# Optimization experiments

Hardware: AMD Instinct MI355X
Metric: run time of the kernel (lower is better)

## Reference

```python
import jax, jax.numpy as jnp
import numpy as np

B, N, C_IN, C_OUT = 4, 2048, 1024, 1024


def setup_inputs() -> dict:
    key = jax.random.key(0)
    ks = jax.random.split(key, 4)
    scale = 1.0 / np.sqrt(C_IN)
    return {
        "hidden_states": jax.random.normal(ks[0], (B, N, C_IN), dtype=jnp.float32),
        "Wq": jax.random.normal(ks[1], (C_OUT, C_IN), dtype=jnp.float32) * scale,
        "bq": jnp.zeros((C_OUT,), dtype=jnp.float32),
        "Wk": jax.random.normal(ks[2], (C_OUT, C_IN), dtype=jnp.float32) * scale,
        "bk": jnp.zeros((C_OUT,), dtype=jnp.float32),
        "Wv": jax.random.normal(ks[3], (C_OUT, C_IN), dtype=jnp.float32) * scale,
        "bv": jnp.zeros((C_OUT,), dtype=jnp.float32),
    }


def reference(hidden_states, Wq, bq, Wk, bk, Wv, bv):
    # torch nn.Linear: y = x @ W.T + b
    Q = jnp.einsum("bnc,dc->bnd", hidden_states, Wq) + bq
    K = jnp.einsum("bnc,dc->bnd", hidden_states, Wk) + bk
    V = jnp.einsum("bnc,dc->bnd", hidden_states, Wv) + bv
    d_k = K.shape[-1]
    scores = jnp.einsum("bnd,bmd->bnm", Q, K) * (d_k ** -0.5)  # [B,N,N]
    attention = jax.nn.softmax(scores, axis=-1)
    out = jnp.einsum("bnm,bmd->bnd", attention, V)
    return (out, attention)
```

## Files before the change

### kernel.cpp

```cpp
#include <hip/hip_runtime.h>
#include <cstdint>

typedef __attribute__((ext_vector_type(8))) short bf16x8;
typedef __attribute__((ext_vector_type(4))) float f32x4;

__device__ __forceinline__ unsigned short f2bf(float v) {
  unsigned u = __builtin_bit_cast(unsigned, v);
  u += 0x7FFFu + ((u >> 16) & 1u);
  return (unsigned short)(u >> 16);
}

__device__ __forceinline__ void gload16(const unsigned short* g, unsigned short* l) {
  __builtin_amdgcn_global_load_lds(
      (const __attribute__((address_space(1))) void*)(uintptr_t)g,
      (__attribute__((address_space(3))) void*)(uint32_t)(uintptr_t)l,
      16, 0, 0);
}

__device__ __forceinline__ void gemm_core(
    const unsigned short* __restrict__ A, const unsigned short* __restrict__ B,
    int lda, int ldb, int K,
    unsigned short* ldsA, unsigned short* ldsB, f32x4 acc[4][4])
{
  const int tid  = threadIdx.x;
  const int wave = tid >> 6;
  const int lane = tid & 63;
  const int wm = (wave >> 1) * 64;
  const int wn = (wave & 1) * 64;
  const int lrow = lane & 15;
  const int kq = lane >> 4;

  const int sr = lane >> 3;
  const int sc = (lane & 7) ^ (sr & 7);
  const unsigned short* ga = A + (long)(wave * 32 + sr) * lda + sc * 8;
  const unsigned short* gb = B + (long)(wave * 32 + sr) * ldb + sc * 8;
  unsigned short* lA = ldsA + wave * 2048;
  unsigned short* lB = ldsB + wave * 2048;

  const int pc0 = ((0 * 4 + kq) ^ (lrow & 7)) * 8;
  const int pc1 = ((1 * 4 + kq) ^ (lrow & 7)) * 8;

#pragma unroll 1
  for (int kb = 0; kb < K; kb += 64) {
    __syncthreads();
#pragma unroll
    for (int i = 0; i < 4; ++i) {
      gload16(ga + kb + (long)i * 8 * lda, lA + i * 512);
      gload16(gb + kb + (long)i * 8 * ldb, lB + i * 512);
    }
    __syncthreads();

    bf16x8 af[4], bfr[4];
#pragma unroll
    for (int i = 0; i < 4; ++i)
      af[i] = *(const bf16x8*)(ldsA + (wm + i * 16 + lrow) * 64 + pc0);
#pragma unroll
    for (int j = 0; j < 4; ++j)
      bfr[j] = *(const bf16x8*)(ldsB + (wn + j * 16 + lrow) * 64 + pc0);
#pragma unroll
    for (int i = 0; i < 4; ++i)
#pragma unroll
      for (int j = 0; j < 4; ++j)
        acc[i][j] = __builtin_amdgcn_mfma_f32_16x16x32_bf16(af[i], bfr[j], acc[i][j], 0, 0, 0);

#pragma unroll
    for (int i = 0; i < 4; ++i)
      af[i] = *(const bf16x8*)(ldsA + (wm + i * 16 + lrow) * 64 + pc1);
#pragma unroll
    for (int j = 0; j < 4; ++j)
      bfr[j] = *(const bf16x8*)(ldsB + (wn + j * 16 + lrow) * 64 + pc1);
#pragma unroll
    for (int i = 0; i < 4; ++i)
#pragma unroll
      for (int j = 0; j < 4; ++j)
        acc[i][j] = __builtin_amdgcn_mfma_f32_16x16x32_bf16(af[i], bfr[j], acc[i][j], 0, 0, 0);
  }
}

__global__ __launch_bounds__(256, 4) void gemm_qkv(
    const unsigned short* __restrict__ xh,
    const unsigned short* __restrict__ wh,
    const float* __restrict__ bq, const float* __restrict__ bk, const float* __restrict__ bv,
    unsigned short* __restrict__ Qh, unsigned short* __restrict__ Kh,
    unsigned short* __restrict__ Vth)
{
  __shared__ __align__(16) unsigned short ldsA[8192];
  __shared__ __align__(16) unsigned short ldsB[8192];
  const int Mblk = blockIdx.x * 128;
  const int sel  = blockIdx.y >> 3;
  const int nb   = blockIdx.y & 7;

  const unsigned short* A = xh + (long)Mblk * 1024;
  const unsigned short* B = wh + sel * 1048576 + (long)(nb * 128) * 1024;
  const float* bias = (sel == 0) ? bq : (sel == 1) ? bk : bv;

  f32x4 acc[4][4] = {};
  gemm_core(A, B, 1024, 1024, 1024, ldsA, ldsB, acc);

  const int lane = threadIdx.x & 63, wave = threadIdx.x >> 6;
  const int wm = (wave >> 1) * 64, wn = (wave & 1) * 64;
  const int lrow = lane & 15, kq = lane >> 4;

#pragma unroll
  for (int i = 0; i < 4; ++i) {
#pragma unroll
    for (int j = 0; j < 4; ++j) {
      const int col = nb * 128 + wn + j * 16 + lrow;
      const float bsv = bias[col];
#pragma unroll
      for (int r = 0; r < 4; ++r) {
        const int tok = Mblk + wm + i * 16 + kq * 4 + r;
        const unsigned short h = f2bf(acc[i][j][r] + bsv);
        if (sel == 2) {
          Vth[(long)(tok >> 11) * 2097152 + (long)col * 2048 + (tok & 2047)] = h;
        } else if (sel == 0) {
          Qh[(long)tok * 1024 + col] = h;
        } else {
          Kh[(long)tok * 1024 + col] = h;
        }
      }
    }
  }
}

__global__ __launch_bounds__(256, 4) void gemm_f32out(
    const unsigned short* __restrict__ A, const unsigned short* __restrict__ B,
    int lda, int ldb, int K,
    long sA, long sB, float* __restrict__ C, int ldc, long sC, float alpha)
{
  __shared__ __align__(16) unsigned short ldsA[8192];
  __shared__ __align__(16) unsigned short ldsB[8192];
  const int Mblk = blockIdx.x * 128;
  const int Nblk = blockIdx.y * 128;
  const long z = blockIdx.z;
  const unsigned short* Ab = A + z * sA + (long)Mblk * lda;
  const unsigned short* Bb = B + z * sB + (long)Nblk * ldb;
  float* Cb = C + z * sC;

  f32x4 acc[4][4] = {};
  gemm_core(Ab, Bb, lda, ldb, K, ldsA, ldsB, acc);

  const int lane = threadIdx.x & 63, wave = threadIdx.x >> 6;
  const int wm = (wave >> 1) * 64, wn = (wave & 1) * 64;
  const int lrow = lane & 15, kq = lane >> 4;
#pragma unroll
  for (int i = 0; i < 4; ++i)
#pragma unroll
    for (int j = 0; j < 4; ++j)
#pragma unroll
      for (int r = 0; r < 4; ++r) {
        const int row = Mblk + wm + i * 16 + kq * 4 + r;
        const int col = Nblk + wn + j * 16 + lrow;
        Cb[(long)row * ldc + col] = alpha * acc[i][j][r];
      }
}

__global__ __launch_bounds__(256) void softmax_rows(
    float* __restrict__ S, unsigned short* __restrict__ Ph)
{
  __shared__ float red[4];
  const long row = blockIdx.x;
  float* rp = S + row * 2048;
  const int t = threadIdx.x;

  float x[8];
  *(float4*)&x[0] = reinterpret_cast<const float4*>(rp)[t];
  *(float4*)&x[4] = reinterpret_cast<const float4*>(rp)[t + 256];

  float m = x[0];
#pragma unroll
  for (int i = 1; i < 8; ++i) m = fmaxf(m, x[i]);
  for (int o = 32; o; o >>= 1) m = fmaxf(m, __shfl_xor(m, o, 64));
  if ((t & 63) == 0) red[t >> 6] = m;
  __syncthreads();
  m = fmaxf(fmaxf(red[0], red[1]), fmaxf(red[2], red[3]));
  __syncthreads();

  float s = 0.f;
#pragma unroll
  for (int i = 0; i < 8; ++i) { x[i] = expf(x[i] - m); s += x[i]; }
  for (int o = 32; o; o >>= 1) s += __shfl_xor(s, o, 64);
  if ((t & 63) == 0) red[t >> 6] = s;
  __syncthreads();
  s = (red[0] + red[1]) + (red[2] + red[3]);
  const float inv = 1.0f / s;

#pragma unroll
  for (int i = 0; i < 8; ++i) x[i] *= inv;
  reinterpret_cast<float4*>(rp)[t]       = *(float4*)&x[0];
  reinterpret_cast<float4*>(rp)[t + 256] = *(float4*)&x[4];

  const long b0 = row * 2048 + t * 4;
#pragma unroll
  for (int k = 0; k < 4; ++k) Ph[b0 + k] = f2bf(x[k]);
  const long b1 = row * 2048 + 1024 + t * 4;
#pragma unroll
  for (int k = 0; k < 4; ++k) Ph[b1 + k] = f2bf(x[4 + k]);
}

__global__ __launch_bounds__(256) void to_bf16(
    const float* __restrict__ x, unsigned short* __restrict__ hi, int n)
{
  int i = blockIdx.x * 256 + threadIdx.x;
  const int stride = gridDim.x * 256;
  for (; i < n; i += stride) hi[i] = f2bf(x[i]);
}

extern "C" void kernel_launch(void* const* d_in, const int* in_sizes, int n_in,
                              void* d_out, int out_size, void* d_ws, size_t ws_size,
                              hipStream_t stream)
{
  const float* x  = (const float*)d_in[0];
  const float* Wq = (const float*)d_in[1];
  const float* bq = (const float*)d_in[2];
  const float* Wk = (const float*)d_in[3];
  const float* bk = (const float*)d_in[4];
  const float* Wv = (const float*)d_in[5];
  const float* bv = (const float*)d_in[6];

  float* out  = (float*)d_out;
  float* attn = (float*)d_out + 8388608;

  unsigned short* ws  = (unsigned short*)d_ws;
  unsigned short* xh  = ws;
  unsigned short* wh  = xh + 8388608;
  unsigned short* Qh  = wh + 3145728;
  unsigned short* Kh  = Qh + 8388608;
  unsigned short* Vth = Kh + 8388608;
  unsigned short* Ph  = Vth + 8388608;

  to_bf16<<<4096, 256, 0, stream>>>(x, xh, 8388608);
  to_bf16<<<512, 256, 0, stream>>>(Wq, wh, 1048576);
  to_bf16<<<512, 256, 0, stream>>>(Wk, wh + 1048576, 1048576);
  to_bf16<<<512, 256, 0, stream>>>(Wv, wh + 2097152, 1048576);

  gemm_qkv<<<dim3(64, 24), 256, 0, stream>>>(xh, wh, bq, bk, bv, Qh, Kh, Vth);

  gemm_f32out<<<dim3(16, 16, 4), 256, 0, stream>>>(Qh, Kh, 1024, 1024, 1024,
      2097152L, 2097152L, attn, 2048, 4194304L, 0.03125f);

  softmax_rows<<<8192, 256, 0, stream>>>(attn, Ph);

  gemm_f32out<<<dim3(16, 8, 4), 256, 0, stream>>>(Ph, Vth, 2048, 2048, 2048,
      4194304L, 2097152L, out, 1024, 2097152L, 1.0f);
}
```

Measured before the change: 314.2 us.

## Rewrite GEMM core as 8-wave 128x256 tile with double-buffered LDS prefetch

Replaces the 4-wave 128x128 GEMM core with an 8-wave 128x256 block tile. It uses a double-buffered LDS pipeline where global-to-LDS loads for the next A and B tiles are issued while MFMAs run on the current tile, with manual vmcnt waits, raw barriers and setprio around the MFMA bursts. This is meant to hide global load latency that the old load/sync/compute loop exposed, and to raise reuse per block. The bf16 conversion kernel is also vectorised to float4 loads. It raises LDS use (96KB per block) and relies on hand-placed waitcnt and barriers, so any ordering mistake risks races; there are also fewer blocks per launch.

Result: slower. 321.6 us (+2.3%).

```diff
diff --git a/kernel.cpp b/kernel.cpp
--- a/kernel.cpp
+++ b/kernel.cpp
@@ -17,99 +17,145 @@
       16, 0, 0);
 }
 
+#define BAR()   asm volatile("s_barrier" ::: "memory")
+#define LGKM0() asm volatile("s_waitcnt lgkmcnt(0)" ::: "memory")
+#define VM4()   asm volatile("s_waitcnt vmcnt(4)" ::: "memory")
+#define VM0()   asm volatile("s_waitcnt vmcnt(0)" ::: "memory")
+
 __device__ __forceinline__ void gemm_core(
     const unsigned short* __restrict__ A, const unsigned short* __restrict__ B,
-    int lda, int ldb, int K,
-    unsigned short* ldsA, unsigned short* ldsB, f32x4 acc[4][4])
+    int lda, int ldb, int NT,
+    unsigned short* lds, f32x4 acc[4][4])
 {
   const int tid  = threadIdx.x;
-  const int wave = tid >> 6;
+  const int w    = tid >> 6;
   const int lane = tid & 63;
-  const int wm = (wave >> 1) * 64;
-  const int wn = (wave & 1) * 64;
+  const int wr   = w >> 2;
+  const int wc   = w & 3;
   const int lrow = lane & 15;
-  const int kq = lane >> 4;
-
-  const int sr = lane >> 3;
-  const int sc = (lane & 7) ^ (sr & 7);
-  const unsigned short* ga = A + (long)(wave * 32 + sr) * lda + sc * 8;
-  const unsigned short* gb = B + (long)(wave * 32 + sr) * ldb + sc * 8;
-  unsigned short* lA = ldsA + wave * 2048;
-  unsigned short* lB = ldsB + wave * 2048;
-
-  const int pc0 = ((0 * 4 + kq) ^ (lrow & 7)) * 8;
-  const int pc1 = ((1 * 4 + kq) ^ (lrow & 7)) * 8;
-
-#pragma unroll 1
-  for (int kb = 0; kb < K; kb += 64) {
-    __syncthreads();
-#pragma unroll
-    for (int i = 0; i < 4; ++i) {
-      gload16(ga + kb + (long)i * 8 * lda, lA + i * 512);
-      gload16(gb + kb + (long)i * 8 * ldb, lB + i * 512);
-    }
-    __syncthreads();
-
-    bf16x8 af[4], bfr[4];
-#pragma unroll
-    for (int i = 0; i < 4; ++i)
-      af[i] = *(const bf16x8*)(ldsA + (wm + i * 16 + lrow) * 64 + pc0);
-#pragma unroll
-    for (int j = 0; j < 4; ++j)
-      bfr[j] = *(const bf16x8*)(ldsB + (wn + j * 16 + lrow) * 64 + pc0);
-#pragma unroll
-    for (int i = 0; i < 4; ++i)
-#pragma unroll
-      for (int j = 0; j < 4; ++j)
-        acc[i][j] = __builtin_amdgcn_mfma_f32_16x16x32_bf16(af[i], bfr[j], acc[i][j], 0, 0, 0);
-
-#pragma unroll
-    for (int i = 0; i < 4; ++i)
-      af[i] = *(const bf16x8*)(ldsA + (wm + i * 16 + lrow) * 64 + pc1);
-#pragma unroll
-    for (int j = 0; j < 4; ++j)
-      bfr[j] = *(const bf16x8*)(ldsB + (wn + j * 16 + lrow) * 64 + pc1);
-#pragma unroll
-    for (int i = 0; i < 4; ++i)
-#pragma unroll
-      for (int j = 0; j < 4; ++j)
-        acc[i][j] = __builtin_amdgcn_mfma_f32_16x16x32_bf16(af[i], bfr[j], acc[i][j], 0, 0, 0);
+  const int kq   = lane >> 4;
+
+  const int srow = tid >> 3;
+  const int schk = ((tid & 7) ^ (srow & 7)) * 8;
+  const unsigned short* gA = A + (long)srow * lda + schk;
+  const unsigned short* gB = B + (long)srow * ldb + schk;
+  unsigned short* const stg = lds + w * 512;
+
+  const int aoff  = (wr * 64 + lrow) * 64;
+  const int boff  = ((wc & 1) * 64 + lrow) * 64;
+  const int bunit = wc >> 1;
+  const int pc0 = ((0 + kq) ^ (lrow & 7)) * 8;
+  const int pc1 = ((4 + kq) ^ (lrow & 7)) * 8;
+
+  gload16(const_cast<unsigned short*>(gB) - 0,          stg);
+  gload16(const_cast<unsigned short*>(gB) + (long)64 * ldb,  stg + 4096);
+  gload16(const_cast<unsigned short*>(gB) + (long)128 * ldb, stg + 8192);
+  gload16(const_cast<unsigned short*>(gB) + (long)192 * ldb, stg + 8192 + 4096);
+  gload16(const_cast<unsigned short*>(gA),                   stg + 2 * 8192);
+  gload16(const_cast<unsigned short*>(gA) + (long)64 * lda,  stg + 2 * 8192 + 4096);
+  gload16(const_cast<unsigned short*>(gB) + 64,              stg + 3 * 8192);
+  gload16(const_cast<unsigned short*>(gB) + 64 + (long)64 * ldb,  stg + 3 * 8192 + 4096);
+  gload16(const_cast<unsigned short*>(gB) + 64 + (long)128 * ldb, stg + 4 * 8192);
+  gload16(const_cast<unsigned short*>(gB) + 64 + (long)192 * ldb, stg + 4 * 8192 + 4096);
+  VM4();
+  BAR();
+
+  for (int t = 0; t < NT; ++t) {
+    const int r3 = 3 * (t & 1);
+    const unsigned short* lA = lds + (r3 + 2) * 8192 + aoff;
+    const unsigned short* lB = lds + (r3 + bunit) * 8192 + boff;
+
+    bf16x8 bfr[4][2], af[2][2];
+#pragma unroll
+    for (int j = 0; j < 4; ++j) {
+      bfr[j][0] = *(const bf16x8*)(lB + j * 1024 + pc0);
+      bfr[j][1] = *(const bf16x8*)(lB + j * 1024 + pc1);
+    }
+#pragma unroll
+    for (int i = 0; i < 2; ++i) {
+      af[i][0] = *(const bf16x8*)(lA + i * 1024 + pc0);
+      af[i][1] = *(const bf16x8*)(lA + i * 1024 + pc1);
+    }
+    if (t + 1 < NT) {
+      const unsigned short* s = gA + (t + 1) * 64;
+      unsigned short* d = stg + (3 * ((t + 1) & 1) + 2) * 8192;
+      gload16(const_cast<unsigned short*>(s),                  d);
+      gload16(const_cast<unsigned short*>(s) + (long)64 * lda, d + 4096);
+    }
+    BAR();
+    LGKM0();
+    __builtin_amdgcn_s_setprio(1);
+#pragma unroll
+    for (int i = 0; i < 2; ++i)
+#pragma unroll
+      for (int j = 0; j < 4; ++j) {
+        acc[i][j] = __builtin_amdgcn_mfma_f32_16x16x32_bf16(af[i][0], bfr[j][0], acc[i][j], 0, 0, 0);
+        acc[i][j] = __builtin_amdgcn_mfma_f32_16x16x32_bf16(af[i][1], bfr[j][1], acc[i][j], 0, 0, 0);
+      }
+    __builtin_amdgcn_s_setprio(0);
+    BAR();
+
+#pragma unroll
+    for (int i = 0; i < 2; ++i) {
+      af[i][0] = *(const bf16x8*)(lA + (i + 2) * 1024 + pc0);
+      af[i][1] = *(const bf16x8*)(lA + (i + 2) * 1024 + pc1);
+    }
+    if (t + 2 < NT) {
+      const unsigned short* s = gB + (t + 2) * 64;
+      unsigned short* d = stg + r3 * 8192;
+      gload16(const_cast<unsigned short*>(s),                   d);
+      gload16(const_cast<unsigned short*>(s) + (long)64 * ldb,  d + 4096);
+      gload16(const_cast<unsigned short*>(s) + (long)128 * ldb, d + 8192);
+      gload16(const_cast<unsigned short*>(s) + (long)192 * ldb, d + 8192 + 4096);
+    }
+    BAR();
+    LGKM0();
+    __builtin_amdgcn_s_setprio(1);
+#pragma unroll
+    for (int i = 0; i < 2; ++i)
+#pragma unroll
+      for (int j = 0; j < 4; ++j) {
+        acc[i + 2][j] = __builtin_amdgcn_mfma_f32_16x16x32_bf16(af[i][0], bfr[j][0], acc[i + 2][j], 0, 0, 0);
+        acc[i + 2][j] = __builtin_amdgcn_mfma_f32_16x16x32_bf16(af[i][1], bfr[j][1], acc[i + 2][j], 0, 0, 0);
+      }
+    __builtin_amdgcn_s_setprio(0);
+    if (t == NT - 2) { VM0(); } else { VM4(); }
+    BAR();
   }
 }
 
-__global__ __launch_bounds__(256, 4) void gemm_qkv(
+__global__ __launch_bounds__(512, 2) void gemm_qkv(
     const unsigned short* __restrict__ xh,
     const unsigned short* __restrict__ wh,
     const float* __restrict__ bq, const float* __restrict__ bk, const float* __restrict__ bv,
     unsigned short* __restrict__ Qh, unsigned short* __restrict__ Kh,
     unsigned short* __restrict__ Vth)
 {
-  __shared__ __align__(16) unsigned short ldsA[8192];
-  __shared__ __align__(16) unsigned short ldsB[8192];
+  __shared__ __align__(16) unsigned short lds[49152];
   const int Mblk = blockIdx.x * 128;
-  const int sel  = blockIdx.y >> 3;
-  const int nb   = blockIdx.y & 7;
+  const int sel  = blockIdx.y >> 2;
+  const int nb   = blockIdx.y & 3;
 
   const unsigned short* A = xh + (long)Mblk * 1024;
-  const unsigned short* B = wh + sel * 1048576 + (long)(nb * 128) * 1024;
+  const unsigned short* B = wh + sel * 1048576 + (long)(nb * 256) * 1024;
   const float* bias = (sel == 0) ? bq : (sel == 1) ? bk : bv;
 
   f32x4 acc[4][4] = {};
-  gemm_core(A, B, 1024, 1024, 1024, ldsA, ldsB, acc);
-
-  const int lane = threadIdx.x & 63, wave = threadIdx.x >> 6;
-  const int wm = (wave >> 1) * 64, wn = (wave & 1) * 64;
+  gemm_core(A, B, 1024, 1024, 16, lds, acc);
+
+  const int lane = threadIdx.x & 63, w = threadIdx.x >> 6;
+  const int wr = w >> 2, wc = w & 3;
   const int lrow = lane & 15, kq = lane >> 4;
 
 #pragma unroll
   for (int i = 0; i < 4; ++i) {
 #pragma unroll
     for (int j = 0; j < 4; ++j) {
-      const int col = nb * 128 + wn + j * 16 + lrow;
+      const int col = nb * 256 + wc * 64 + j * 16 + lrow;
       const float bsv = bias[col];
 #pragma unroll
       for (int r = 0; r < 4; ++r) {
-        const int tok = Mblk + wm + i * 16 + kq * 4 + r;
+        const int tok = Mblk + wr * 64 + i * 16 + kq * 4 + r;
         const unsigned short h = f2bf(acc[i][j][r] + bsv);
         if (sel == 2) {
           Vth[(long)(tok >> 11) * 2097152 + (long)col * 2048 + (tok & 2047)] = h;
@@ -123,25 +169,24 @@
   }
 }
 
-__global__ __launch_bounds__(256, 4) void gemm_f32out(
+__global__ __launch_bounds__(512, 2) void gemm_f32out(
     const unsigned short* __restrict__ A, const unsigned short* __restrict__ B,
-    int lda, int ldb, int K,
+    int lda, int ldb, int NT,
     long sA, long sB, float* __restrict__ C, int ldc, long sC, float alpha)
 {
-  __shared__ __align__(16) unsigned short ldsA[8192];
-  __shared__ __align__(16) unsigned short ldsB[8192];
+  __shared__ __align__(16) unsigned short lds[49152];
   const int Mblk = blockIdx.x * 128;
-  const int Nblk = blockIdx.y * 128;
+  const int Nblk = blockIdx.y * 256;
   const long z = blockIdx.z;
   const unsigned short* Ab = A + z * sA + (long)Mblk * lda;
   const unsigned short* Bb = B + z * sB + (long)Nblk * ldb;
   float* Cb = C + z * sC;
 
   f32x4 acc[4][4] = {};
-  gemm_core(Ab, Bb, lda, ldb, K, ldsA, ldsB, acc);
-
-  const int lane = threadIdx.x & 63, wave = threadIdx.x >> 6;
-  const int wm = (wave >> 1) * 64, wn = (wave & 1) * 64;
+  gemm_core(Ab, Bb, lda, ldb, NT, lds, acc);
+
+  const int lane = threadIdx.x & 63, w = threadIdx.x >> 6;
+  const int wr = w >> 2, wc = w & 3;
   const int lrow = lane & 15, kq = lane >> 4;
 #pragma unroll
   for (int i = 0; i < 4; ++i)
@@ -149,8 +194,8 @@
     for (int j = 0; j < 4; ++j)
 #pragma unroll
       for (int r = 0; r < 4; ++r) {
-        const int row = Mblk + wm + i * 16 + kq * 4 + r;
-        const int col = Nblk + wn + j * 16 + lrow;
+        const int row = Mblk + wr * 64 + i * 16 + kq * 4 + r;
+        const int col = Nblk + wc * 64 + j * 16 + lrow;
         Cb[(long)row * ldc + col] = alpha * acc[i][j][r];
       }
 }
@@ -199,11 +244,16 @@
 }
 
 __global__ __launch_bounds__(256) void to_bf16(
-    const float* __restrict__ x, unsigned short* __restrict__ hi, int n)
+    const float* __restrict__ x, unsigned short* __restrict__ hi, int n4)
 {
   int i = blockIdx.x * 256 + threadIdx.x;
   const int stride = gridDim.x * 256;
-  for (; i < n; i += stride) hi[i] = f2bf(x[i]);
+  for (; i < n4; i += stride) {
+    const float4 v = reinterpret_cast<const float4*>(x)[i];
+    ushort4 h;
+    h.x = f2bf(v.x); h.y = f2bf(v.y); h.z = f2bf(v.z); h.w = f2bf(v.w);
+    reinterpret_cast<ushort4*>(hi)[i] = h;
+  }
 }
 
 extern "C" void kernel_launch(void* const* d_in, const int* in_sizes, int n_in,
@@ -229,18 +279,18 @@
   unsigned short* Vth = Kh + 8388608;
   unsigned short* Ph  = Vth + 8388608;
 
-  to_bf16<<<4096, 256, 0, stream>>>(x, xh, 8388608);
-  to_bf16<<<512, 256, 0, stream>>>(Wq, wh, 1048576);
-  to_bf16<<<512, 256, 0, stream>>>(Wk, wh + 1048576, 1048576);
-  to_bf16<<<512, 256, 0, stream>>>(Wv, wh + 2097152, 1048576);
-
-  gemm_qkv<<<dim3(64, 24), 256, 0, stream>>>(xh, wh, bq, bk, bv, Qh, Kh, Vth);
-
-  gemm_f32out<<<dim3(16, 16, 4), 256, 0, stream>>>(Qh, Kh, 1024, 1024, 1024,
+  to_bf16<<<2048, 256, 0, stream>>>(x, xh, 2097152);
+  to_bf16<<<512, 256, 0, stream>>>(Wq, wh, 262144);
+  to_bf16<<<512, 256, 0, stream>>>(Wk, wh + 1048576, 262144);
+  to_bf16<<<512, 256, 0, stream>>>(Wv, wh + 2097152, 262144);
+
+  gemm_qkv<<<dim3(64, 12), 512, 0, stream>>>(xh, wh, bq, bk, bv, Qh, Kh, Vth);
+
+  gemm_f32out<<<dim3(16, 8, 4), 512, 0, stream>>>(Qh, Kh, 1024, 1024, 16,
       2097152L, 2097152L, attn, 2048, 4194304L, 0.03125f);
 
   softmax_rows<<<8192, 256, 0, stream>>>(attn, Ph);
 
-  gemm_f32out<<<dim3(16, 8, 4), 256, 0, stream>>>(Ph, Vth, 2048, 2048, 2048,
+  gemm_f32out<<<dim3(16, 4, 4), 512, 0, stream>>>(Ph, Vth, 2048, 2048, 32,
       4194304L, 2097152L, out, 1024, 2097152L, 1.0f);
 }
```
